# Kernel tuning notes

Hardware: AMD Instinct MI355X
Metric: run time of the kernel (lower is better)

Reference implementation:

```python
import jax, jax.numpy as jnp
import numpy as np

B = 16384      # batch
E = 128        # embed_dim
H = 256        # hidden_dim
OUT = 2        # output_dim
S = 32         # seq_length (decoder steps)
CAR = 8        # car_num


def setup_inputs() -> dict:
    key = jax.random.key(0)
    ks = jax.random.split(key, 17)
    def rn(k, shape, s=0.05):
        return jax.random.normal(k, shape, dtype=jnp.float32) * s
    return {
        "x": rn(ks[0], (B, 6 + CAR * 6), 1.0),
        "emb_mt_W": rn(ks[1], (E, 6)), "emb_mt_b": rn(ks[2], (E,)),
        "emb_v_W": rn(ks[3], (E, 6)), "emb_v_b": rn(ks[4], (E,)),
        "enc_Wih": rn(ks[5], (3 * H, E)), "enc_Whh": rn(ks[6], (3 * H, H)),
        "enc_bih": rn(ks[7], (3 * H,)), "enc_bhh": rn(ks[8], (3 * H,)),
        "dec_Wih": rn(ks[9], (3 * H, H)), "dec_Whh": rn(ks[10], (3 * H, H)),
        "dec_bih": rn(ks[11], (3 * H,)), "dec_bhh": rn(ks[12], (3 * H,)),
        "fc1_W": rn(ks[13], (H, H)), "fc1_b": rn(ks[14], (H,)),
        "fc2_W": rn(ks[15], (OUT, H)), "fc2_b": rn(ks[16], (OUT,)),
    }


def gru_cell(x, h, Wih, Whh, bih, bhh):
    # PyTorch GRU cell: r,z,n gate order
    gi = x @ Wih.T + bih          # [B, 3H]
    gh = h @ Whh.T + bhh          # [B, 3H]
    ir, iz, inn = jnp.split(gi, 3, axis=-1)
    hr, hz, hn = jnp.split(gh, 3, axis=-1)
    r = jax.nn.sigmoid(ir + hr)
    z = jax.nn.sigmoid(iz + hz)
    n = jnp.tanh(inn + r * hn)
    return (1.0 - z) * n + z * h


def reference(x, emb_mt_W, emb_mt_b, emb_v_W, emb_v_b,
              enc_Wih, enc_Whh, enc_bih, enc_bhh,
              dec_Wih, dec_Whh, dec_bih, dec_bhh,
              fc1_W, fc1_b, fc2_W, fc2_b):
    main_target = x[:, :6]                                  # [B,6]
    vehicles = x[:, 6:6 + CAR * 6].reshape(-1, CAR, 6)      # [B,CAR,6]
    # NOTE: original applies a random permutation over the CAR axis
    # (torch.randperm); we use the identity permutation for determinism,
    # the per-element math is identical.
    mt_emb = main_target @ emb_mt_W.T + emb_mt_b            # [B,E]
    v_emb = vehicles @ emb_v_W.T + emb_v_b                  # [B,CAR,E]
    seq = jnp.tanh(jnp.concatenate([v_emb, mt_emb[:, None, :]], axis=1))  # [B,CAR+1,E]

    h0 = jnp.zeros((x.shape[0], H), dtype=x.dtype)
    def enc_step(h, xt):
        return gru_cell(xt, h, enc_Wih, enc_Whh, enc_bih, enc_bhh), None
    h_enc, _ = jax.lax.scan(enc_step, h0, jnp.swapaxes(seq, 0, 1))  # [B,H]

    # decoder_input = encoder_output[:, -1] == final hidden (1-layer GRU)
    def dec_step(carry, _):
        dec_in, h = carry
        h = gru_cell(dec_in, h, dec_Wih, dec_Whh, dec_bih, dec_bhh)
        y = jnp.tanh(jax.nn.relu(h @ fc1_W.T + fc1_b) @ fc2_W.T + fc2_b)  # [B,OUT]
        return (h, h), y
    _, ys = jax.lax.scan(dec_step, (h_enc, h_enc), None, length=S)  # [S,B,OUT]
    return jnp.swapaxes(ys, 0, 1)  # [B,S,OUT]
```

## Files before the change

### kernel.cpp

```cpp
#include <hip/hip_runtime.h>
#include <math.h>
#include <stdint.h>

typedef _Float16 f16;
typedef _Float16 f16x8 __attribute__((ext_vector_type(8)));
typedef float    f32x16 __attribute__((ext_vector_type(16)));

#define NBLK 256
#define NTHR 512
#define MROW 64

#define ENCS 640
#define FC2S 1216
#define TOT_F 1232
#define TOT_E (TOT_F*512)

#define MFMA32(a,b,c) __builtin_amdgcn_mfma_f32_32x32x16_f16((a),(b),(c),0,0,0)
#define VMW4()  asm volatile("s_waitcnt vmcnt(4)" ::: "memory")
#define LGKM0() asm volatile("s_waitcnt lgkmcnt(0)" ::: "memory")
#define BARR()  do { __builtin_amdgcn_s_barrier(); asm volatile("" ::: "memory"); } while(0)

__device__ __forceinline__ void gld16(const f16* g, f16* lds){
  __builtin_amdgcn_global_load_lds(
      (const __attribute__((address_space(1))) void*)(uintptr_t)(const void*)g,
      (__attribute__((address_space(3))) void*)(uint32_t)(uintptr_t)(void*)lds,
      16, 0, 0);
}

__device__ __forceinline__ float sigm(float v){
  return __fdividef(1.0f, 1.0f + __expf(-v));
}
__device__ __forceinline__ float tanh_f(float v){
  float t = fminf(v, 8.0f);
  float e = __expf(2.0f * t);
  return 1.0f - 2.0f * __fdividef(1.0f, e + 1.0f);
}
__device__ __forceinline__ int eX(int row, int k){ return row*128 + (k ^ ((row & 7) << 3)); }

__global__ void prep_pack(const float* __restrict__ eWih, const float* __restrict__ eWhh,
                          const float* __restrict__ dWih, const float* __restrict__ dWhh,
                          const float* __restrict__ f1W,  const float* __restrict__ f2W,
                          f16* __restrict__ ws16)
{
  int idx = blockIdx.x * 256 + threadIdx.x;
  if (idx >= TOT_E) return;
  int frag = idx >> 9;
  int lo   = idx & 511;
  int l    = lo >> 3;
  int jj   = lo & 7;
  int c32  = l & 31;
  int half = l >> 5;
  int kin  = half*8 + jj;
  float v = 0.0f;
  if (frag < ENCS){
    int ct = frag / 80, r80 = frag % 80, n = r80 >> 1, j = r80 & 1;
    int col = ct*32 + c32;
    if (n < 16){ int k = n*16 + kin;
      v = (j == 0) ? (dWih[col*256 + k]       + dWhh[col*256 + k])
                   : (dWih[(256+col)*256 + k] + dWhh[(256+col)*256 + k]);
    } else if (n < 32){ int k = (n-16)*16 + kin;
      v = (j == 0) ? dWih[(512+col)*256 + k] : dWhh[(512+col)*256 + k];
    } else { int ks = (n-32)*2 + j; int k = ks*16 + kin;
      v = f1W[col*256 + k];
    }
  } else if (frag < FC2S){
    int f = frag - ENCS;
    int ct = f / 72, r = f % 72, n = r >> 1, j = r & 1;
    int col = ct*32 + c32;
    if (n < 8)       { int k = n*16 + kin;       v = eWih[(j*256 + col)*128 + k]; }
    else if (n < 24) { int k = (n-8)*16 + kin;   v = eWhh[(j*256 + col)*256 + k]; }
    else if (n < 28) { int ks = (n-24)*2 + j;    v = eWih[(512 + col)*128 + ks*16 + kin]; }
    else             { int ks = (n-28)*2 + j;    v = eWhh[(512 + col)*256 + ks*16 + kin]; }
  } else {
    int ks = frag - FC2S; int k = ks*16 + kin;
    v = (c32 < 2) ? f2W[c32*256 + k] : 0.0f;
  }
  ws16[idx] = (f16)v;
}

__global__ __launch_bounds__(NTHR, 1)
void fused_net(const float* __restrict__ x,
               const float* __restrict__ emW, const float* __restrict__ emb_,
               const float* __restrict__ evW, const float* __restrict__ evb,
               const float* __restrict__ ebih, const float* __restrict__ ebhh,
               const float* __restrict__ dbih, const float* __restrict__ dbhh,
               const float* __restrict__ f1b, const float* __restrict__ f2b,
               const f16* __restrict__ ws16, float* __restrict__ out)
{
  __shared__ __align__(16) f16 H0[16384];
  __shared__ __align__(16) f16 H1[16384];
  __shared__ __align__(16) f16 stg[32768];
  __shared__ __align__(16) f16 xbuf[8192];

  const int tid  = threadIdx.x;
  const int r0   = blockIdx.x * MROW;
  const int l    = tid & 63;
  const int wu   = __builtin_amdgcn_readfirstlane(tid >> 6);
  const int c32  = l & 31;
  const int half = l >> 5;
  const int lo8  = l << 3;

  f16* hp = H0;
  f16* hq = H1;

  const int abase = c32*256 + ((half*8) ^ ((l & 7) << 3));
  const int xab   = c32*128 + ((half*8) ^ ((l & 7) << 3));
  const int colm  = wu*32 + c32;

  f16* slot0 = stg + wu*4096;

  const f16* gdec = ws16 + (size_t)(wu*80)*512          + lo8;
  const f16* genc = ws16 + (size_t)(ENCS + wu*72)*512   + lo8;
  const f16* gfc2 = ws16 + (size_t)FC2S*512             + lo8;

  auto issue = [&](const f16* sb, int n, int q){
    f16* d = slot0 + q*1024;
    const f16* g = sb + (size_t)n*1024;
    gld16(g, d);
    gld16(g + 512, d + 512);
  };

  issue(genc, 0, 0); issue(genc, 1, 1); issue(genc, 2, 2);

  for (int i = tid; i < 16384; i += NTHR) H0[i] = (f16)0.0f;

  {
    const float ebr = ebih[colm]       + ebhh[colm];
    const float ebz = ebih[256 + colm] + ebhh[256 + colm];
    const float ebn = ebih[512 + colm];
    const float ebh = ebhh[512 + colm];

    #pragma unroll 1
    for (int t = 0; t < 9; ++t){
      const bool tlt8 = (t < 8);
      {
        int e  = tid & 127;
        int rq = tid >> 7;
        const float* Wp = tlt8 ? (evW + e*6) : (emW + e*6);
        float bb = tlt8 ? evb[e] : emb_[e];
        float w0 = Wp[0], w1 = Wp[1], w2 = Wp[2], w3 = Wp[3], w4 = Wp[4], w5 = Wp[5];
        int xo = tlt8 ? (6 + t*6) : 0;
        #pragma unroll 1
        for (int rr = 0; rr < 16; ++rr){
          int row = rq*16 + rr;
          const float* xs = x + (size_t)(r0 + row)*54 + xo;
          float a = bb + xs[0]*w0 + xs[1]*w1 + xs[2]*w2 + xs[3]*w3 + xs[4]*w4 + xs[5]*w5;
          xbuf[eX(row, e)] = (f16)tanh_f(a);
        }
      }
      LGKM0(); BARR();

      f32x16 rvv[2], zvv[2];
      {
        f32x16 aR[2], aZ[2];
        aR[0]=0.f; aR[1]=0.f; aZ[0]=0.f; aZ[1]=0.f;
        #pragma unroll 4
        for (int u = 0; u < 24; ++u){
          VMW4();
          issue(genc, u + 3, (u + 3) & 3);
          const f16* sp = slot0 + (u & 3)*1024;
          f16x8 b0 = *(const f16x8*)(sp + lo8);
          f16x8 b1 = *(const f16x8*)(sp + 512 + lo8);
          if (u < 8){
            int ao = xab ^ (u << 4);
            f16x8 a0 = *(const f16x8*)(xbuf + ao);
            f16x8 a1 = *(const f16x8*)(xbuf + ao + 4096);
            aR[0]=MFMA32(a0,b0,aR[0]); aR[1]=MFMA32(a1,b0,aR[1]);
            aZ[0]=MFMA32(a0,b1,aZ[0]); aZ[1]=MFMA32(a1,b1,aZ[1]);
          } else {
            int ao = abase ^ ((u - 8) << 4);
            f16x8 a0 = *(const f16x8*)(hp + ao);
            f16x8 a1 = *(const f16x8*)(hp + ao + 8192);
            aR[0]=MFMA32(a0,b0,aR[0]); aR[1]=MFMA32(a1,b0,aR[1]);
            aZ[0]=MFMA32(a0,b1,aZ[0]); aZ[1]=MFMA32(a1,b1,aZ[1]);
          }
        }
        #pragma unroll
        for (int rt = 0; rt < 2; ++rt)
          #pragma unroll
          for (int rg = 0; rg < 16; ++rg){
            rvv[rt][rg] = sigm(aR[rt][rg] + ebr);
            zvv[rt][rg] = sigm(aZ[rt][rg] + ebz);
          }
      }
      {
        f32x16 aN[2], aH[2];
        aN[0]=0.f; aN[1]=0.f; aH[0]=0.f; aH[1]=0.f;
        #pragma unroll
        for (int m = 0; m < 12; ++m){
          int u = 24 + m;
          VMW4();
          int nn = u + 3;
          if (nn < 36)      issue(genc, nn, nn & 3);
          else if (tlt8)    issue(genc, nn - 36, nn & 3);
          else              issue(gdec, nn - 36, nn & 3);
          const f16* sp = slot0 + (u & 3)*1024;
          f16x8 b0 = *(const f16x8*)(sp + lo8);
          f16x8 b1 = *(const f16x8*)(sp + 512 + lo8);
          if (m < 4){
            int j = 2*m;
            int ao0 = xab ^ (j << 4), ao1 = xab ^ ((j+1) << 4);
            f16x8 a0 = *(const f16x8*)(xbuf + ao0);
            f16x8 a1 = *(const f16x8*)(xbuf + ao0 + 4096);
            aN[0]=MFMA32(a0,b0,aN[0]); aN[1]=MFMA32(a1,b0,aN[1]);
            f16x8 a2 = *(const f16x8*)(xbuf + ao1);
            f16x8 a3 = *(const f16x8*)(xbuf + ao1 + 4096);
            aN[0]=MFMA32(a2,b1,aN[0]); aN[1]=MFMA32(a3,b1,aN[1]);
          } else {
            int k = 2*(m-4);
            int ao0 = abase ^ (k << 4), ao1 = abase ^ ((k+1) << 4);
            f16x8 a0 = *(const f16x8*)(hp + ao0);
            f16x8 a1 = *(const f16x8*)(hp + ao0 + 8192);
            aH[0]=MFMA32(a0,b0,aH[0]); aH[1]=MFMA32(a1,b0,aH[1]);
            f16x8 a2 = *(const f16x8*)(hp + ao1);
            f16x8 a3 = *(const f16x8*)(hp + ao1 + 8192);
            aH[0]=MFMA32(a2,b1,aH[0]); aH[1]=MFMA32(a3,b1,aH[1]);
          }
        }
        #pragma unroll
        for (int rt = 0; rt < 2; ++rt){
          #pragma unroll
          for (int rg = 0; rg < 16; ++rg){
            int rr  = (rg & 3) + 8*(rg >> 2) + 4*half;
            int row = rt*32 + rr;
            int el  = row*256 + (colm ^ ((rr & 7) << 3));
            float nv = tanh_f(aN[rt][rg] + ebn + rvv[rt][rg]*(aH[rt][rg] + ebh));
            float ho = (float)hp[el];
            hq[el] = (f16)(nv + zvv[rt][rg]*(ho - nv));
          }
        }
      }
      LGKM0(); BARR();
      { f16* tmp = hp; hp = hq; hq = tmp; }
    }
  }

  const float dbr = dbih[colm]       + dbhh[colm];
  const float dbz = dbih[256 + colm] + dbhh[256 + colm];
  const float dbn = dbih[512 + colm];
  const float dbh = dbhh[512 + colm];
  const float f1bb = f1b[colm];
  const float f2bb = (c32 < 2) ? f2b[c32] : 0.0f;

  #pragma unroll 1
  for (int s = 0; s < 32; ++s){
    f32x16 rvv[2], zvv[2];
    {
      f32x16 aR[2], aZ[2];
      aR[0]=0.f; aR[1]=0.f; aZ[0]=0.f; aZ[1]=0.f;
      #pragma unroll 4
      for (int u = 0; u < 16; ++u){
        VMW4();
        issue(gdec, u + 3, (u + 3) & 3);
        const f16* sp = slot0 + (u & 3)*1024;
        f16x8 b0 = *(const f16x8*)(sp + lo8);
        f16x8 b1 = *(const f16x8*)(sp + 512 + lo8);
        int ao = abase ^ (u << 4);
        f16x8 a0 = *(const f16x8*)(hp + ao);
        f16x8 a1 = *(const f16x8*)(hp + ao + 8192);
        aR[0]=MFMA32(a0,b0,aR[0]); aR[1]=MFMA32(a1,b0,aR[1]);
        aZ[0]=MFMA32(a0,b1,aZ[0]); aZ[1]=MFMA32(a1,b1,aZ[1]);
      }
      #pragma unroll
      for (int rt = 0; rt < 2; ++rt)
        #pragma unroll
        for (int rg = 0; rg < 16; ++rg){
          rvv[rt][rg] = sigm(aR[rt][rg] + dbr);
          zvv[rt][rg] = sigm(aZ[rt][rg] + dbz);
        }
    }
    BARR();

    {
      f32x16 aN[2], aH[2];
      aN[0]=0.f; aN[1]=0.f; aH[0]=0.f; aH[1]=0.f;
      #pragma unroll 4
      for (int u = 16; u < 32; ++u){
        VMW4();
        issue(gdec, u + 3, (u + 3) & 3);
        const f16* sp = slot0 + (u & 3)*1024;
        f16x8 b0 = *(const f16x8*)(sp + lo8);
        f16x8 b1 = *(const f16x8*)(sp + 512 + lo8);
        int k = u - 16;
        int ao = abase ^ (k << 4);
        f16x8 a0 = *(const f16x8*)(hp + ao);
        f16x8 a1 = *(const f16x8*)(hp + ao + 8192);
        aN[0]=MFMA32(a0,b0,aN[0]); aN[1]=MFMA32(a1,b0,aN[1]);
        aH[0]=MFMA32(a0,b1,aH[0]); aH[1]=MFMA32(a1,b1,aH[1]);
      }
      #pragma unroll
      for (int rt = 0; rt < 2; ++rt){
        #pragma unroll
        for (int rg = 0; rg < 16; ++rg){
          int rr  = (rg & 3) + 8*(rg >> 2) + 4*half;
          int row = rt*32 + rr;
          int el  = row*256 + (colm ^ ((rr & 7) << 3));
          float nv = tanh_f(aN[rt][rg] + dbn + rvv[rt][rg]*(aH[rt][rg] + dbh));
          float ho = (float)hp[el];
          hq[el] = (f16)(nv + zvv[rt][rg]*(ho - nv));
        }
      }
    }
    LGKM0(); BARR();

    {
      f32x16 aF[2];
      aF[0]=0.f; aF[1]=0.f;
      #pragma unroll
      for (int f = 0; f < 8; ++f){
        VMW4();
        int nn = 35 + f;
        if (nn < 40) issue(gdec, nn, nn & 3);
        else         issue(gdec, nn - 40, nn & 3);
        const f16* sp = slot0 + (f & 3)*1024;
        f16x8 b0 = *(const f16x8*)(sp + lo8);
        f16x8 b1 = *(const f16x8*)(sp + 512 + lo8);
        int k0 = 2*f;
        int ao0 = abase ^ (k0 << 4), ao1 = abase ^ ((k0+1) << 4);
        f16x8 a0 = *(const f16x8*)(hq + ao0);
        f16x8 a1 = *(const f16x8*)(hq + ao0 + 8192);
        aF[0]=MFMA32(a0,b0,aF[0]); aF[1]=MFMA32(a1,b0,aF[1]);
        f16x8 a2 = *(const f16x8*)(hq + ao1);
        f16x8 a3 = *(const f16x8*)(hq + ao1 + 8192);
        aF[0]=MFMA32(a2,b1,aF[0]); aF[1]=MFMA32(a3,b1,aF[1]);
      }
      #pragma unroll
      for (int rt = 0; rt < 2; ++rt){
        #pragma unroll
        for (int rg = 0; rg < 16; ++rg){
          int rr  = (rg & 3) + 8*(rg >> 2) + 4*half;
          int row = rt*32 + rr;
          int el  = row*256 + (colm ^ ((rr & 7) << 3));
          hp[el] = (f16)fmaxf(aF[rt][rg] + f1bb, 0.0f);
        }
      }
    }
    LGKM0(); BARR();

    if (wu < 2){
      f32x16 a2 = 0.f;
      const int rb = wu * 8192;
      #pragma unroll
      for (int ks = 0; ks < 16; ++ks){
        f16x8 bv = *(const f16x8*)(gfc2 + (size_t)ks*512);
        f16x8 a0 = *(const f16x8*)(hp + ((abase + rb) ^ (ks << 4)));
        a2 = MFMA32(a0, bv, a2);
      }
      if (c32 < 2){
        #pragma unroll
        for (int rg = 0; rg < 16; ++rg){
          int rr = (rg & 3) + 8*(rg >> 2) + 4*half;
          out[((size_t)(r0 + wu*32 + rr)*32 + s)*2 + c32] = tanh_f(a2[rg] + f2bb);
        }
      }
    }
    { f16* tmp = hp; hp = hq; hq = tmp; }
  }
}

extern "C" void kernel_launch(void* const* d_in, const int* in_sizes, int n_in,
                              void* d_out, int out_size, void* d_ws, size_t ws_size,
                              hipStream_t stream)
{
  (void)in_sizes; (void)n_in; (void)out_size; (void)ws_size;
  const float* x    = (const float*)d_in[0];
  const float* emW  = (const float*)d_in[1];
  const float* emb_ = (const float*)d_in[2];
  const float* evW  = (const float*)d_in[3];
  const float* evb  = (const float*)d_in[4];
  const float* eWih = (const float*)d_in[5];
  const float* eWhh = (const float*)d_in[6];
  const float* ebih = (const float*)d_in[7];
  const float* ebhh = (const float*)d_in[8];
  const float* dWih = (const float*)d_in[9];
  const float* dWhh = (const float*)d_in[10];
  const float* dbih = (const float*)d_in[11];
  const float* dbhh = (const float*)d_in[12];
  const float* f1W  = (const float*)d_in[13];
  const float* f1b  = (const float*)d_in[14];
  const float* f2W  = (const float*)d_in[15];
  const float* f2b  = (const float*)d_in[16];
  float* out = (float*)d_out;
  f16* ws16 = (f16*)d_ws;

  prep_pack<<<(TOT_E + 255)/256, 256, 0, stream>>>(eWih, eWhh, dWih, dWhh, f1W, f2W, ws16);
  fused_net<<<NBLK, NTHR, 0, stream>>>(x, emW, emb_, evW, evb, ebih, ebhh,
                                       dbih, dbhh, f1b, f2b, ws16, out);
}
```

Before: 748.4 us.

## Halve rows per block, shrink LDS, triple-buffer weight staging for multi-block occupancy

Rows per block go from 64 to 32 and the grid doubles to 512 blocks, with launch bounds raised so several blocks can share a CU. LDS use shrinks: the hidden buffers are halved, the separate x buffer is dropped by reusing the spare hidden buffer for embedded inputs, and the weight staging ring goes from four slots to three with a rotating pointer set. Each MFMA step now uses a single 32-row accumulator, and the next weight slice is issued only after the LDS reads (lgkmcnt wait). The intent is to hide latency through more resident waves. The cost is that every block now streams the full weight set for half as many rows, so weight traffic through L2 doubles, and the extra barrier in the encoder step plus the three-slot rotation add synchronization hazards.

New measurement: 2.341 ms. 3.13x slower.

```diff
diff --git a/kernel.cpp b/kernel.cpp
--- a/kernel.cpp
+++ b/kernel.cpp
@@ -6,9 +6,9 @@
 typedef _Float16 f16x8 __attribute__((ext_vector_type(8)));
 typedef float    f32x16 __attribute__((ext_vector_type(16)));
 
-#define NBLK 256
+#define NBLK 512
 #define NTHR 512
-#define MROW 64
+#define MROW 32
 
 #define ENCS 640
 #define FC2S 1216
@@ -78,7 +78,7 @@
   ws16[idx] = (f16)v;
 }
 
-__global__ __launch_bounds__(NTHR, 1)
+__global__ __launch_bounds__(NTHR, 4)
 void fused_net(const float* __restrict__ x,
                const float* __restrict__ emW, const float* __restrict__ emb_,
                const float* __restrict__ evW, const float* __restrict__ evb,
@@ -87,10 +87,9 @@
                const float* __restrict__ f1b, const float* __restrict__ f2b,
                const f16* __restrict__ ws16, float* __restrict__ out)
 {
-  __shared__ __align__(16) f16 H0[16384];
-  __shared__ __align__(16) f16 H1[16384];
-  __shared__ __align__(16) f16 stg[32768];
-  __shared__ __align__(16) f16 xbuf[8192];
+  __shared__ __align__(16) f16 H0[8192];
+  __shared__ __align__(16) f16 H1[8192];
+  __shared__ __align__(16) f16 stg[24576];
 
   const int tid  = threadIdx.x;
   const int r0   = blockIdx.x * MROW;
@@ -107,22 +106,22 @@
   const int xab   = c32*128 + ((half*8) ^ ((l & 7) << 3));
   const int colm  = wu*32 + c32;
 
-  f16* slot0 = stg + wu*4096;
+  f16* spp[3];
+  spp[0] = stg + wu*3072;
+  spp[1] = spp[0] + 1024;
+  spp[2] = spp[0] + 2048;
 
   const f16* gdec = ws16 + (size_t)(wu*80)*512          + lo8;
   const f16* genc = ws16 + (size_t)(ENCS + wu*72)*512   + lo8;
   const f16* gfc2 = ws16 + (size_t)FC2S*512             + lo8;
 
-  auto issue = [&](const f16* sb, int n, int q){
-    f16* d = slot0 + q*1024;
-    const f16* g = sb + (size_t)n*1024;
-    gld16(g, d);
-    gld16(g + 512, d + 512);
-  };
-
-  issue(genc, 0, 0); issue(genc, 1, 1); issue(genc, 2, 2);
-
-  for (int i = tid; i < 16384; i += NTHR) H0[i] = (f16)0.0f;
+  {
+    gld16(genc,            spp[0]); gld16(genc + 512,           spp[0] + 512);
+    gld16(genc + 1024,     spp[1]); gld16(genc + 1536,          spp[1] + 512);
+    gld16(genc + 2048,     spp[2]); gld16(genc + 2560,          spp[2] + 512);
+  }
+
+  for (int i = tid; i < 8192; i += NTHR) H0[i] = (f16)0.0f;
 
   {
     const float ebr = ebih[colm]       + ebhh[colm];
@@ -133,6 +132,7 @@
     #pragma unroll 1
     for (int t = 0; t < 9; ++t){
       const bool tlt8 = (t < 8);
+      f16* xb = hq;
       {
         int e  = tid & 127;
         int rq = tid >> 7;
@@ -141,93 +141,86 @@
         float w0 = Wp[0], w1 = Wp[1], w2 = Wp[2], w3 = Wp[3], w4 = Wp[4], w5 = Wp[5];
         int xo = tlt8 ? (6 + t*6) : 0;
         #pragma unroll 1
-        for (int rr = 0; rr < 16; ++rr){
-          int row = rq*16 + rr;
+        for (int rr = 0; rr < 8; ++rr){
+          int row = rq*8 + rr;
           const float* xs = x + (size_t)(r0 + row)*54 + xo;
           float a = bb + xs[0]*w0 + xs[1]*w1 + xs[2]*w2 + xs[3]*w3 + xs[4]*w4 + xs[5]*w5;
-          xbuf[eX(row, e)] = (f16)tanh_f(a);
+          xb[eX(row, e)] = (f16)tanh_f(a);
         }
       }
       LGKM0(); BARR();
 
-      f32x16 rvv[2], zvv[2];
+      f32x16 rvv, zvv;
       {
-        f32x16 aR[2], aZ[2];
-        aR[0]=0.f; aR[1]=0.f; aZ[0]=0.f; aZ[1]=0.f;
-        #pragma unroll 4
+        f32x16 aR = 0.f, aZ = 0.f;
+        #pragma unroll
         for (int u = 0; u < 24; ++u){
           VMW4();
-          issue(genc, u + 3, (u + 3) & 3);
-          const f16* sp = slot0 + (u & 3)*1024;
+          f16* sp = spp[u % 3];
           f16x8 b0 = *(const f16x8*)(sp + lo8);
           f16x8 b1 = *(const f16x8*)(sp + 512 + lo8);
-          if (u < 8){
-            int ao = xab ^ (u << 4);
-            f16x8 a0 = *(const f16x8*)(xbuf + ao);
-            f16x8 a1 = *(const f16x8*)(xbuf + ao + 4096);
-            aR[0]=MFMA32(a0,b0,aR[0]); aR[1]=MFMA32(a1,b0,aR[1]);
-            aZ[0]=MFMA32(a0,b1,aZ[0]); aZ[1]=MFMA32(a1,b1,aZ[1]);
-          } else {
-            int ao = abase ^ ((u - 8) << 4);
-            f16x8 a0 = *(const f16x8*)(hp + ao);
-            f16x8 a1 = *(const f16x8*)(hp + ao + 8192);
-            aR[0]=MFMA32(a0,b0,aR[0]); aR[1]=MFMA32(a1,b0,aR[1]);
-            aZ[0]=MFMA32(a0,b1,aZ[0]); aZ[1]=MFMA32(a1,b1,aZ[1]);
-          }
-        }
-        #pragma unroll
-        for (int rt = 0; rt < 2; ++rt)
-          #pragma unroll
-          for (int rg = 0; rg < 16; ++rg){
-            rvv[rt][rg] = sigm(aR[rt][rg] + ebr);
-            zvv[rt][rg] = sigm(aZ[rt][rg] + ebz);
-          }
-      }
+          f16x8 a0 = (u < 8) ? *(const f16x8*)(xb + (xab ^ (u << 4)))
+                             : *(const f16x8*)(hp + (abase ^ ((u - 8) << 4)));
+          LGKM0();
+          { const f16* g = genc + (size_t)(u + 3)*1024;
+            gld16(g, sp); gld16(g + 512, sp + 512); }
+          aR = MFMA32(a0, b0, aR);
+          aZ = MFMA32(a0, b1, aZ);
+        }
+        #pragma unroll
+        for (int rg = 0; rg < 16; ++rg){
+          rvv[rg] = sigm(aR[rg] + ebr);
+          zvv[rg] = sigm(aZ[rg] + ebz);
+        }
+      }
+      f32x16 aN = 0.f, aH = 0.f;
       {
-        f32x16 aN[2], aH[2];
-        aN[0]=0.f; aN[1]=0.f; aH[0]=0.f; aH[1]=0.f;
-        #pragma unroll
-        for (int m = 0; m < 12; ++m){
+        #pragma unroll
+        for (int m = 0; m < 4; ++m){
           int u = 24 + m;
           VMW4();
-          int nn = u + 3;
-          if (nn < 36)      issue(genc, nn, nn & 3);
-          else if (tlt8)    issue(genc, nn - 36, nn & 3);
-          else              issue(gdec, nn - 36, nn & 3);
-          const f16* sp = slot0 + (u & 3)*1024;
+          f16* sp = spp[u % 3];
           f16x8 b0 = *(const f16x8*)(sp + lo8);
           f16x8 b1 = *(const f16x8*)(sp + 512 + lo8);
-          if (m < 4){
-            int j = 2*m;
-            int ao0 = xab ^ (j << 4), ao1 = xab ^ ((j+1) << 4);
-            f16x8 a0 = *(const f16x8*)(xbuf + ao0);
-            f16x8 a1 = *(const f16x8*)(xbuf + ao0 + 4096);
-            aN[0]=MFMA32(a0,b0,aN[0]); aN[1]=MFMA32(a1,b0,aN[1]);
-            f16x8 a2 = *(const f16x8*)(xbuf + ao1);
-            f16x8 a3 = *(const f16x8*)(xbuf + ao1 + 4096);
-            aN[0]=MFMA32(a2,b1,aN[0]); aN[1]=MFMA32(a3,b1,aN[1]);
-          } else {
-            int k = 2*(m-4);
-            int ao0 = abase ^ (k << 4), ao1 = abase ^ ((k+1) << 4);
-            f16x8 a0 = *(const f16x8*)(hp + ao0);
-            f16x8 a1 = *(const f16x8*)(hp + ao0 + 8192);
-            aH[0]=MFMA32(a0,b0,aH[0]); aH[1]=MFMA32(a1,b0,aH[1]);
-            f16x8 a2 = *(const f16x8*)(hp + ao1);
-            f16x8 a3 = *(const f16x8*)(hp + ao1 + 8192);
-            aH[0]=MFMA32(a2,b1,aH[0]); aH[1]=MFMA32(a3,b1,aH[1]);
-          }
-        }
-        #pragma unroll
-        for (int rt = 0; rt < 2; ++rt){
-          #pragma unroll
-          for (int rg = 0; rg < 16; ++rg){
-            int rr  = (rg & 3) + 8*(rg >> 2) + 4*half;
-            int row = rt*32 + rr;
-            int el  = row*256 + (colm ^ ((rr & 7) << 3));
-            float nv = tanh_f(aN[rt][rg] + ebn + rvv[rt][rg]*(aH[rt][rg] + ebh));
-            float ho = (float)hp[el];
-            hq[el] = (f16)(nv + zvv[rt][rg]*(ho - nv));
-          }
+          int j = 2*m;
+          f16x8 a0 = *(const f16x8*)(xb + (xab ^ (j << 4)));
+          f16x8 a1 = *(const f16x8*)(xb + (xab ^ ((j + 1) << 4)));
+          LGKM0();
+          { const f16* g = genc + (size_t)(u + 3)*1024;
+            gld16(g, sp); gld16(g + 512, sp + 512); }
+          aN = MFMA32(a0, b0, aN);
+          aN = MFMA32(a1, b1, aN);
+        }
+      }
+      LGKM0(); BARR();
+      {
+        #pragma unroll
+        for (int m = 4; m < 12; ++m){
+          int u = 24 + m;
+          VMW4();
+          f16* sp = spp[u % 3];
+          f16x8 b0 = *(const f16x8*)(sp + lo8);
+          f16x8 b1 = *(const f16x8*)(sp + 512 + lo8);
+          int k = 2*(m - 4);
+          f16x8 a0 = *(const f16x8*)(hp + (abase ^ (k << 4)));
+          f16x8 a1 = *(const f16x8*)(hp + (abase ^ ((k + 1) << 4)));
+          LGKM0();
+          { int nn = u + 3;
+            const f16* g;
+            if (nn < 36)      g = genc + (size_t)nn*1024;
+            else if (tlt8)    g = genc + (size_t)(nn - 36)*1024;
+            else              g = gdec + (size_t)(nn - 36)*1024;
+            gld16(g, sp); gld16(g + 512, sp + 512); }
+          aH = MFMA32(a0, b0, aH);
+          aH = MFMA32(a1, b1, aH);
+        }
+        #pragma unroll
+        for (int rg = 0; rg < 16; ++rg){
+          int rr = (rg & 3) + 8*(rg >> 2) + 4*half;
+          int el = rr*256 + (colm ^ ((rr & 7) << 3));
+          float nv = tanh_f(aN[rg] + ebn + rvv[rg]*(aH[rg] + ebh));
+          float ho = (float)hp[el];
+          hq[el] = (f16)(nv + zvv[rg]*(ho - nv));
         }
       }
       LGKM0(); BARR();
@@ -244,116 +237,99 @@
 
   #pragma unroll 1
   for (int s = 0; s < 32; ++s){
-    f32x16 rvv[2], zvv[2];
+    f32x16 rvv, zvv;
     {
-      f32x16 aR[2], aZ[2];
-      aR[0]=0.f; aR[1]=0.f; aZ[0]=0.f; aZ[1]=0.f;
-      #pragma unroll 4
+      f32x16 aR = 0.f, aZ = 0.f;
+      #pragma unroll
       for (int u = 0; u < 16; ++u){
         VMW4();
-        issue(gdec, u + 3, (u + 3) & 3);
-        const f16* sp = slot0 + (u & 3)*1024;
+        f16* sp = spp[u % 3];
         f16x8 b0 = *(const f16x8*)(sp + lo8);
         f16x8 b1 = *(const f16x8*)(sp + 512 + lo8);
-        int ao = abase ^ (u << 4);
-        f16x8 a0 = *(const f16x8*)(hp + ao);
-        f16x8 a1 = *(const f16x8*)(hp + ao + 8192);
-        aR[0]=MFMA32(a0,b0,aR[0]); aR[1]=MFMA32(a1,b0,aR[1]);
-        aZ[0]=MFMA32(a0,b1,aZ[0]); aZ[1]=MFMA32(a1,b1,aZ[1]);
-      }
-      #pragma unroll
-      for (int rt = 0; rt < 2; ++rt)
-        #pragma unroll
-        for (int rg = 0; rg < 16; ++rg){
-          rvv[rt][rg] = sigm(aR[rt][rg] + dbr);
-          zvv[rt][rg] = sigm(aZ[rt][rg] + dbz);
-        }
+        f16x8 a0 = *(const f16x8*)(hp + (abase ^ (u << 4)));
+        LGKM0();
+        { const f16* g = gdec + (size_t)(u + 3)*1024;
+          gld16(g, sp); gld16(g + 512, sp + 512); }
+        aR = MFMA32(a0, b0, aR);
+        aZ = MFMA32(a0, b1, aZ);
+      }
+      #pragma unroll
+      for (int rg = 0; rg < 16; ++rg){
+        rvv[rg] = sigm(aR[rg] + dbr);
+        zvv[rg] = sigm(aZ[rg] + dbz);
+      }
     }
     BARR();
 
     {
-      f32x16 aN[2], aH[2];
-      aN[0]=0.f; aN[1]=0.f; aH[0]=0.f; aH[1]=0.f;
-      #pragma unroll 4
+      f32x16 aN = 0.f, aH = 0.f;
+      #pragma unroll
       for (int u = 16; u < 32; ++u){
         VMW4();
-        issue(gdec, u + 3, (u + 3) & 3);
-        const f16* sp = slot0 + (u & 3)*1024;
+        f16* sp = spp[u % 3];
         f16x8 b0 = *(const f16x8*)(sp + lo8);
         f16x8 b1 = *(const f16x8*)(sp + 512 + lo8);
-        int k = u - 16;
-        int ao = abase ^ (k << 4);
-        f16x8 a0 = *(const f16x8*)(hp + ao);
-        f16x8 a1 = *(const f16x8*)(hp + ao + 8192);
-        aN[0]=MFMA32(a0,b0,aN[0]); aN[1]=MFMA32(a1,b0,aN[1]);
-        aH[0]=MFMA32(a0,b1,aH[0]); aH[1]=MFMA32(a1,b1,aH[1]);
-      }
-      #pragma unroll
-      for (int rt = 0; rt < 2; ++rt){
-        #pragma unroll
-        for (int rg = 0; rg < 16; ++rg){
-          int rr  = (rg & 3) + 8*(rg >> 2) + 4*half;
-          int row = rt*32 + rr;
-          int el  = row*256 + (colm ^ ((rr & 7) << 3));
-          float nv = tanh_f(aN[rt][rg] + dbn + rvv[rt][rg]*(aH[rt][rg] + dbh));
-          float ho = (float)hp[el];
-          hq[el] = (f16)(nv + zvv[rt][rg]*(ho - nv));
-        }
+        f16x8 a0 = *(const f16x8*)(hp + (abase ^ ((u - 16) << 4)));
+        LGKM0();
+        { const f16* g = gdec + (size_t)(u + 3)*1024;
+          gld16(g, sp); gld16(g + 512, sp + 512); }
+        aN = MFMA32(a0, b0, aN);
+        aH = MFMA32(a0, b1, aH);
+      }
+      #pragma unroll
+      for (int rg = 0; rg < 16; ++rg){
+        int rr = (rg & 3) + 8*(rg >> 2) + 4*half;
+        int el = rr*256 + (colm ^ ((rr & 7) << 3));
+        float nv = tanh_f(aN[rg] + dbn + rvv[rg]*(aH[rg] + dbh));
+        float ho = (float)hp[el];
+        hq[el] = (f16)(nv + zvv[rg]*(ho - nv));
       }
     }
     LGKM0(); BARR();
 
     {
-      f32x16 aF[2];
-      aF[0]=0.f; aF[1]=0.f;
-      #pragma unroll
-      for (int f = 0; f < 8; ++f){
+      f32x16 aF = 0.f;
+      #pragma unroll
+      for (int u = 32; u < 40; ++u){
         VMW4();
-        int nn = 35 + f;
-        if (nn < 40) issue(gdec, nn, nn & 3);
-        else         issue(gdec, nn - 40, nn & 3);
-        const f16* sp = slot0 + (f & 3)*1024;
+        f16* sp = spp[u % 3];
         f16x8 b0 = *(const f16x8*)(sp + lo8);
         f16x8 b1 = *(const f16x8*)(sp + 512 + lo8);
-        int k0 = 2*f;
-        int ao0 = abase ^ (k0 << 4), ao1 = abase ^ ((k0+1) << 4);
-        f16x8 a0 = *(const f16x8*)(hq + ao0);
-        f16x8 a1 = *(const f16x8*)(hq + ao0 + 8192);
-        aF[0]=MFMA32(a0,b0,aF[0]); aF[1]=MFMA32(a1,b0,aF[1]);
-        f16x8 a2 = *(const f16x8*)(hq + ao1);
-        f16x8 a3 = *(const f16x8*)(hq + ao1 + 8192);
-        aF[0]=MFMA32(a2,b1,aF[0]); aF[1]=MFMA32(a3,b1,aF[1]);
-      }
-      #pragma unroll
-      for (int rt = 0; rt < 2; ++rt){
-        #pragma unroll
-        for (int rg = 0; rg < 16; ++rg){
-          int rr  = (rg & 3) + 8*(rg >> 2) + 4*half;
-          int row = rt*32 + rr;
-          int el  = row*256 + (colm ^ ((rr & 7) << 3));
-          hp[el] = (f16)fmaxf(aF[rt][rg] + f1bb, 0.0f);
-        }
+        int k0 = 2*(u - 32);
+        f16x8 a0 = *(const f16x8*)(hq + (abase ^ (k0 << 4)));
+        f16x8 a1 = *(const f16x8*)(hq + (abase ^ ((k0 + 1) << 4)));
+        LGKM0();
+        { const f16* g = gdec + (size_t)((u + 3) % 40)*1024;
+          gld16(g, sp); gld16(g + 512, sp + 512); }
+        aF = MFMA32(a0, b0, aF);
+        aF = MFMA32(a1, b1, aF);
+      }
+      #pragma unroll
+      for (int rg = 0; rg < 16; ++rg){
+        int rr = (rg & 3) + 8*(rg >> 2) + 4*half;
+        int el = rr*256 + (colm ^ ((rr & 7) << 3));
+        hp[el] = (f16)fmaxf(aF[rg] + f1bb, 0.0f);
       }
     }
     LGKM0(); BARR();
 
-    if (wu < 2){
+    if (wu == 0){
       f32x16 a2 = 0.f;
-      const int rb = wu * 8192;
       #pragma unroll
       for (int ks = 0; ks < 16; ++ks){
         f16x8 bv = *(const f16x8*)(gfc2 + (size_t)ks*512);
-        f16x8 a0 = *(const f16x8*)(hp + ((abase + rb) ^ (ks << 4)));
+        f16x8 a0 = *(const f16x8*)(hp + (abase ^ (ks << 4)));
         a2 = MFMA32(a0, bv, a2);
       }
       if (c32 < 2){
         #pragma unroll
         for (int rg = 0; rg < 16; ++rg){
           int rr = (rg & 3) + 8*(rg >> 2) + 4*half;
-          out[((size_t)(r0 + wu*32 + rr)*32 + s)*2 + c32] = tanh_f(a2[rg] + f2bb);
-        }
-      }
-    }
+          out[((size_t)(r0 + rr)*32 + s)*2 + c32] = tanh_f(a2[rg] + f2bb);
+        }
+      }
+    }
+    { f16* t0 = spp[0]; spp[0] = spp[1]; spp[1] = spp[2]; spp[2] = t0; }
     { f16* tmp = hp; hp = hq; hq = tmp; }
   }
 }
```

## Deepen weight staging to five slots, pair K-steps, widen LDS swizzle, reuse hq for x

Applied to the files above, without the earlier changes.

Switches the per-wave weight staging ring from four slots to five and processes two K-slices per wait, issuing two prefetches per iteration so more global-to-LDS loads are in flight. Each wait now covers two slices, with the ring rotating across encoder steps. The LDS XOR swizzle widens from 8 to 16 row groups to cut bank conflicts. The separate x buffer is removed and embeddings are written into the idle hq buffer, which adds a barrier before the h-dependent n-gate work. Fully unrolling the loops raises register and code pressure, and the pointer-array ring rotation adds complexity.

Result: slower. 1.838 ms (+145.6%).

```diff
diff --git a/kernel.cpp b/kernel.cpp
--- a/kernel.cpp
+++ b/kernel.cpp
@@ -35,7 +35,7 @@
   float e = __expf(2.0f * t);
   return 1.0f - 2.0f * __fdividef(1.0f, e + 1.0f);
 }
-__device__ __forceinline__ int eX(int row, int k){ return row*128 + (k ^ ((row & 7) << 3)); }
+__device__ __forceinline__ int eX(int row, int k){ return row*128 + (k ^ ((row & 15) << 3)); }
 
 __global__ void prep_pack(const float* __restrict__ eWih, const float* __restrict__ eWhh,
                           const float* __restrict__ dWih, const float* __restrict__ dWhh,
@@ -89,8 +89,7 @@
 {
   __shared__ __align__(16) f16 H0[16384];
   __shared__ __align__(16) f16 H1[16384];
-  __shared__ __align__(16) f16 stg[32768];
-  __shared__ __align__(16) f16 xbuf[8192];
+  __shared__ __align__(16) f16 stg[40960];
 
   const int tid  = threadIdx.x;
   const int r0   = blockIdx.x * MROW;
@@ -103,24 +102,24 @@
   f16* hp = H0;
   f16* hq = H1;
 
-  const int abase = c32*256 + ((half*8) ^ ((l & 7) << 3));
-  const int xab   = c32*128 + ((half*8) ^ ((l & 7) << 3));
+  const int abase = c32*256 + ((half*8) ^ ((l & 15) << 3));
+  const int xab   = c32*128 + ((half*8) ^ ((l & 15) << 3));
   const int colm  = wu*32 + c32;
 
-  f16* slot0 = stg + wu*4096;
+  f16* spp[5];
+  #pragma unroll
+  for (int i = 0; i < 5; ++i) spp[i] = stg + wu*5120 + i*1024;
 
   const f16* gdec = ws16 + (size_t)(wu*80)*512          + lo8;
   const f16* genc = ws16 + (size_t)(ENCS + wu*72)*512   + lo8;
   const f16* gfc2 = ws16 + (size_t)FC2S*512             + lo8;
 
-  auto issue = [&](const f16* sb, int n, int q){
-    f16* d = slot0 + q*1024;
-    const f16* g = sb + (size_t)n*1024;
-    gld16(g, d);
-    gld16(g + 512, d + 512);
-  };
-
-  issue(genc, 0, 0); issue(genc, 1, 1); issue(genc, 2, 2);
+  auto issue2 = [&](const f16* g, f16* d){ gld16(g, d); gld16(g + 512, d + 512); };
+
+  issue2(genc,        spp[0]);
+  issue2(genc + 1024, spp[1]);
+  issue2(genc + 2048, spp[2]);
+  issue2(genc + 3072, spp[3]);
 
   for (int i = tid; i < 16384; i += NTHR) H0[i] = (f16)0.0f;
 
@@ -133,6 +132,7 @@
     #pragma unroll 1
     for (int t = 0; t < 9; ++t){
       const bool tlt8 = (t < 8);
+      f16* xb = hq;
       {
         int e  = tid & 127;
         int rq = tid >> 7;
@@ -145,7 +145,7 @@
           int row = rq*16 + rr;
           const float* xs = x + (size_t)(r0 + row)*54 + xo;
           float a = bb + xs[0]*w0 + xs[1]*w1 + xs[2]*w2 + xs[3]*w3 + xs[4]*w4 + xs[5]*w5;
-          xbuf[eX(row, e)] = (f16)tanh_f(a);
+          xb[eX(row, e)] = (f16)tanh_f(a);
         }
       }
       LGKM0(); BARR();
@@ -154,25 +154,36 @@
       {
         f32x16 aR[2], aZ[2];
         aR[0]=0.f; aR[1]=0.f; aZ[0]=0.f; aZ[1]=0.f;
-        #pragma unroll 4
-        for (int u = 0; u < 24; ++u){
+        #pragma unroll
+        for (int p = 0; p < 12; ++p){
+          const int u0 = 2*p, u1 = 2*p + 1;
           VMW4();
-          issue(genc, u + 3, (u + 3) & 3);
-          const f16* sp = slot0 + (u & 3)*1024;
-          f16x8 b0 = *(const f16x8*)(sp + lo8);
-          f16x8 b1 = *(const f16x8*)(sp + 512 + lo8);
-          if (u < 8){
-            int ao = xab ^ (u << 4);
-            f16x8 a0 = *(const f16x8*)(xbuf + ao);
-            f16x8 a1 = *(const f16x8*)(xbuf + ao + 4096);
-            aR[0]=MFMA32(a0,b0,aR[0]); aR[1]=MFMA32(a1,b0,aR[1]);
-            aZ[0]=MFMA32(a0,b1,aZ[0]); aZ[1]=MFMA32(a1,b1,aZ[1]);
-          } else {
-            int ao = abase ^ ((u - 8) << 4);
-            f16x8 a0 = *(const f16x8*)(hp + ao);
-            f16x8 a1 = *(const f16x8*)(hp + ao + 8192);
-            aR[0]=MFMA32(a0,b0,aR[0]); aR[1]=MFMA32(a1,b0,aR[1]);
-            aZ[0]=MFMA32(a0,b1,aZ[0]); aZ[1]=MFMA32(a1,b1,aZ[1]);
+          f16* s0 = spp[u0 % 5];
+          f16* s1 = spp[u1 % 5];
+          f16x8 b00 = *(const f16x8*)(s0 + lo8);
+          f16x8 b01 = *(const f16x8*)(s0 + 512 + lo8);
+          f16x8 b10 = *(const f16x8*)(s1 + lo8);
+          f16x8 b11 = *(const f16x8*)(s1 + 512 + lo8);
+          issue2(genc + (size_t)(u0 + 4)*1024, spp[(u0 + 4) % 5]);
+          issue2(genc + (size_t)(u1 + 4)*1024, spp[(u1 + 4) % 5]);
+          #pragma unroll
+          for (int q = 0; q < 2; ++q){
+            const int u = q ? u1 : u0;
+            f16x8 b0 = q ? b10 : b00;
+            f16x8 b1 = q ? b11 : b01;
+            if (u < 8){
+              int ao = xab ^ (u << 4);
+              f16x8 a0 = *(const f16x8*)(xb + ao);
+              f16x8 a1 = *(const f16x8*)(xb + ao + 4096);
+              aR[0]=MFMA32(a0,b0,aR[0]); aR[1]=MFMA32(a1,b0,aR[1]);
+              aZ[0]=MFMA32(a0,b1,aZ[0]); aZ[1]=MFMA32(a1,b1,aZ[1]);
+            } else {
+              int ao = abase ^ ((u - 8) << 4);
+              f16x8 a0 = *(const f16x8*)(hp + ao);
+              f16x8 a1 = *(const f16x8*)(hp + ao + 8192);
+              aR[0]=MFMA32(a0,b0,aR[0]); aR[1]=MFMA32(a1,b0,aR[1]);
+              aZ[0]=MFMA32(a0,b1,aZ[0]); aZ[1]=MFMA32(a1,b1,aZ[1]);
+            }
           }
         }
         #pragma unroll
@@ -183,31 +194,64 @@
             zvv[rt][rg] = sigm(aZ[rt][rg] + ebz);
           }
       }
+      f32x16 aN[2], aH[2];
+      aN[0]=0.f; aN[1]=0.f; aH[0]=0.f; aH[1]=0.f;
       {
-        f32x16 aN[2], aH[2];
-        aN[0]=0.f; aN[1]=0.f; aH[0]=0.f; aH[1]=0.f;
-        #pragma unroll
-        for (int m = 0; m < 12; ++m){
-          int u = 24 + m;
+        #pragma unroll
+        for (int p = 12; p < 14; ++p){
+          const int u0 = 2*p, u1 = 2*p + 1;
           VMW4();
-          int nn = u + 3;
-          if (nn < 36)      issue(genc, nn, nn & 3);
-          else if (tlt8)    issue(genc, nn - 36, nn & 3);
-          else              issue(gdec, nn - 36, nn & 3);
-          const f16* sp = slot0 + (u & 3)*1024;
-          f16x8 b0 = *(const f16x8*)(sp + lo8);
-          f16x8 b1 = *(const f16x8*)(sp + 512 + lo8);
-          if (m < 4){
+          f16* s0 = spp[u0 % 5];
+          f16* s1 = spp[u1 % 5];
+          f16x8 b00 = *(const f16x8*)(s0 + lo8);
+          f16x8 b01 = *(const f16x8*)(s0 + 512 + lo8);
+          f16x8 b10 = *(const f16x8*)(s1 + lo8);
+          f16x8 b11 = *(const f16x8*)(s1 + 512 + lo8);
+          issue2(genc + (size_t)(u0 + 4)*1024, spp[(u0 + 4) % 5]);
+          issue2(genc + (size_t)(u1 + 4)*1024, spp[(u1 + 4) % 5]);
+          #pragma unroll
+          for (int q = 0; q < 2; ++q){
+            const int m = (q ? u1 : u0) - 24;
+            f16x8 b0 = q ? b10 : b00;
+            f16x8 b1 = q ? b11 : b01;
             int j = 2*m;
             int ao0 = xab ^ (j << 4), ao1 = xab ^ ((j+1) << 4);
-            f16x8 a0 = *(const f16x8*)(xbuf + ao0);
-            f16x8 a1 = *(const f16x8*)(xbuf + ao0 + 4096);
+            f16x8 a0 = *(const f16x8*)(xb + ao0);
+            f16x8 a1 = *(const f16x8*)(xb + ao0 + 4096);
             aN[0]=MFMA32(a0,b0,aN[0]); aN[1]=MFMA32(a1,b0,aN[1]);
-            f16x8 a2 = *(const f16x8*)(xbuf + ao1);
-            f16x8 a3 = *(const f16x8*)(xbuf + ao1 + 4096);
+            f16x8 a2 = *(const f16x8*)(xb + ao1);
+            f16x8 a3 = *(const f16x8*)(xb + ao1 + 4096);
             aN[0]=MFMA32(a2,b1,aN[0]); aN[1]=MFMA32(a3,b1,aN[1]);
-          } else {
-            int k = 2*(m-4);
+          }
+        }
+      }
+      LGKM0(); BARR();
+      {
+        #pragma unroll
+        for (int p = 14; p < 18; ++p){
+          const int u0 = 2*p, u1 = 2*p + 1;
+          VMW4();
+          f16* s0 = spp[u0 % 5];
+          f16* s1 = spp[u1 % 5];
+          f16x8 b00 = *(const f16x8*)(s0 + lo8);
+          f16x8 b01 = *(const f16x8*)(s0 + 512 + lo8);
+          f16x8 b10 = *(const f16x8*)(s1 + lo8);
+          f16x8 b11 = *(const f16x8*)(s1 + 512 + lo8);
+          {
+            const int n0 = u0 + 4, n1 = u1 + 4;
+            const f16* g0 = (n0 < 36) ? (genc + (size_t)n0*1024)
+                                      : ((tlt8 ? genc : gdec) + (size_t)(n0 - 36)*1024);
+            const f16* g1 = (n1 < 36) ? (genc + (size_t)n1*1024)
+                                      : ((tlt8 ? genc : gdec) + (size_t)(n1 - 36)*1024);
+            issue2(g0, spp[n0 % 5]);
+            issue2(g1, spp[n1 % 5]);
+          }
+          #pragma unroll
+          for (int q = 0; q < 2; ++q){
+            const int m = (q ? u1 : u0) - 24;
+            f16x8 b0 = q ? b10 : b00;
+            f16x8 b1 = q ? b11 : b01;
+            int k = 2*(m - 4);
             int ao0 = abase ^ (k << 4), ao1 = abase ^ ((k+1) << 4);
             f16x8 a0 = *(const f16x8*)(hp + ao0);
             f16x8 a1 = *(const f16x8*)(hp + ao0 + 8192);
@@ -223,7 +267,7 @@
           for (int rg = 0; rg < 16; ++rg){
             int rr  = (rg & 3) + 8*(rg >> 2) + 4*half;
             int row = rt*32 + rr;
-            int el  = row*256 + (colm ^ ((rr & 7) << 3));
+            int el  = row*256 + (colm ^ ((rr & 15) << 3));
             float nv = tanh_f(aN[rt][rg] + ebn + rvv[rt][rg]*(aH[rt][rg] + ebh));
             float ho = (float)hp[el];
             hq[el] = (f16)(nv + zvv[rt][rg]*(ho - nv));
@@ -232,6 +276,7 @@
       }
       LGKM0(); BARR();
       { f16* tmp = hp; hp = hq; hq = tmp; }
+      { f16* t0 = spp[0]; spp[0]=spp[1]; spp[1]=spp[2]; spp[2]=spp[3]; spp[3]=spp[4]; spp[4]=t0; }
     }
   }
 
@@ -248,18 +293,29 @@
     {
       f32x16 aR[2], aZ[2];
       aR[0]=0.f; aR[1]=0.f; aZ[0]=0.f; aZ[1]=0.f;
-      #pragma unroll 4
-      for (int u = 0; u < 16; ++u){
+      #pragma unroll
+      for (int p = 0; p < 8; ++p){
+        const int u0 = 2*p, u1 = 2*p + 1;
         VMW4();
-        issue(gdec, u + 3, (u + 3) & 3);
-        const f16* sp = slot0 + (u & 3)*1024;
-        f16x8 b0 = *(const f16x8*)(sp + lo8);
-        f16x8 b1 = *(const f16x8*)(sp + 512 + lo8);
-        int ao = abase ^ (u << 4);
-        f16x8 a0 = *(const f16x8*)(hp + ao);
-        f16x8 a1 = *(const f16x8*)(hp + ao + 8192);
-        aR[0]=MFMA32(a0,b0,aR[0]); aR[1]=MFMA32(a1,b0,aR[1]);
-        aZ[0]=MFMA32(a0,b1,aZ[0]); aZ[1]=MFMA32(a1,b1,aZ[1]);
+        f16* s0 = spp[u0 % 5];
+        f16* s1 = spp[u1 % 5];
+        f16x8 b00 = *(const f16x8*)(s0 + lo8);
+        f16x8 b01 = *(const f16x8*)(s0 + 512 + lo8);
+        f16x8 b10 = *(const f16x8*)(s1 + lo8);
+        f16x8 b11 = *(const f16x8*)(s1 + 512 + lo8);
+        issue2(gdec + (size_t)(u0 + 4)*1024, spp[(u0 + 4) % 5]);
+        issue2(gdec + (size_t)(u1 + 4)*1024, spp[(u1 + 4) % 5]);
+        #pragma unroll
+        for (int q = 0; q < 2; ++q){
+          const int u = q ? u1 : u0;
+          f16x8 b0 = q ? b10 : b00;
+          f16x8 b1 = q ? b11 : b01;
+          int ao = abase ^ (u << 4);
+          f16x8 a0 = *(const f16x8*)(hp + ao);
+          f16x8 a1 = *(const f16x8*)(hp + ao + 8192);
+          aR[0]=MFMA32(a0,b0,aR[0]); aR[1]=MFMA32(a1,b0,aR[1]);
+          aZ[0]=MFMA32(a0,b1,aZ[0]); aZ[1]=MFMA32(a1,b1,aZ[1]);
+        }
       }
       #pragma unroll
       for (int rt = 0; rt < 2; ++rt)
@@ -274,19 +330,29 @@
     {
       f32x16 aN[2], aH[2];
       aN[0]=0.f; aN[1]=0.f; aH[0]=0.f; aH[1]=0.f;
-      #pragma unroll 4
-      for (int u = 16; u < 32; ++u){
+      #pragma unroll
+      for (int p = 8; p < 16; ++p){
+        const int u0 = 2*p, u1 = 2*p + 1;
         VMW4();
-        issue(gdec, u + 3, (u + 3) & 3);
-        const f16* sp = slot0 + (u & 3)*1024;
-        f16x8 b0 = *(const f16x8*)(sp + lo8);
-        f16x8 b1 = *(const f16x8*)(sp + 512 + lo8);
-        int k = u - 16;
-        int ao = abase ^ (k << 4);
-        f16x8 a0 = *(const f16x8*)(hp + ao);
-        f16x8 a1 = *(const f16x8*)(hp + ao + 8192);
-        aN[0]=MFMA32(a0,b0,aN[0]); aN[1]=MFMA32(a1,b0,aN[1]);
-        aH[0]=MFMA32(a0,b1,aH[0]); aH[1]=MFMA32(a1,b1,aH[1]);
+        f16* s0 = spp[u0 % 5];
+        f16* s1 = spp[u1 % 5];
+        f16x8 b00 = *(const f16x8*)(s0 + lo8);
+        f16x8 b01 = *(const f16x8*)(s0 + 512 + lo8);
+        f16x8 b10 = *(const f16x8*)(s1 + lo8);
+        f16x8 b11 = *(const f16x8*)(s1 + 512 + lo8);
+        issue2(gdec + (size_t)(u0 + 4)*1024, spp[(u0 + 4) % 5]);
+        issue2(gdec + (size_t)(u1 + 4)*1024, spp[(u1 + 4) % 5]);
+        #pragma unroll
+        for (int q = 0; q < 2; ++q){
+          const int u = q ? u1 : u0;
+          f16x8 b0 = q ? b10 : b00;
+          f16x8 b1 = q ? b11 : b01;
+          int ao = abase ^ ((u - 16) << 4);
+          f16x8 a0 = *(const f16x8*)(hp + ao);
+          f16x8 a1 = *(const f16x8*)(hp + ao + 8192);
+          aN[0]=MFMA32(a0,b0,aN[0]); aN[1]=MFMA32(a1,b0,aN[1]);
+          aH[0]=MFMA32(a0,b1,aH[0]); aH[1]=MFMA32(a1,b1,aH[1]);
+        }
       }
       #pragma unroll
       for (int rt = 0; rt < 2; ++rt){
@@ -294,7 +360,7 @@
         for (int rg = 0; rg < 16; ++rg){
           int rr  = (rg & 3) + 8*(rg >> 2) + 4*half;
           int row = rt*32 + rr;
-          int el  = row*256 + (colm ^ ((rr & 7) << 3));
+          int el  = row*256 + (colm ^ ((rr & 15) << 3));
           float nv = tanh_f(aN[rt][rg] + dbn + rvv[rt][rg]*(aH[rt][rg] + dbh));
           float ho = (float)hp[el];
           hq[el] = (f16)(nv + zvv[rt][rg]*(ho - nv));
@@ -307,22 +373,36 @@
       f32x16 aF[2];
       aF[0]=0.f; aF[1]=0.f;
       #pragma unroll
-      for (int f = 0; f < 8; ++f){
+      for (int p = 16; p < 20; ++p){
+        const int u0 = 2*p, u1 = 2*p + 1;
         VMW4();
-        int nn = 35 + f;
-        if (nn < 40) issue(gdec, nn, nn & 3);
-        else         issue(gdec, nn - 40, nn & 3);
-        const f16* sp = slot0 + (f & 3)*1024;
-        f16x8 b0 = *(const f16x8*)(sp + lo8);
-        f16x8 b1 = *(const f16x8*)(sp + 512 + lo8);
-        int k0 = 2*f;
-        int ao0 = abase ^ (k0 << 4), ao1 = abase ^ ((k0+1) << 4);
-        f16x8 a0 = *(const f16x8*)(hq + ao0);
-        f16x8 a1 = *(const f16x8*)(hq + ao0 + 8192);
-        aF[0]=MFMA32(a0,b0,aF[0]); aF[1]=MFMA32(a1,b0,aF[1]);
-        f16x8 a2 = *(const f16x8*)(hq + ao1);
-        f16x8 a3 = *(const f16x8*)(hq + ao1 + 8192);
-        aF[0]=MFMA32(a2,b1,aF[0]); aF[1]=MFMA32(a3,b1,aF[1]);
+        f16* s0 = spp[u0 % 5];
+        f16* s1 = spp[u1 % 5];
+        f16x8 b00 = *(const f16x8*)(s0 + lo8);
+        f16x8 b01 = *(const f16x8*)(s0 + 512 + lo8);
+        f16x8 b10 = *(const f16x8*)(s1 + lo8);
+        f16x8 b11 = *(const f16x8*)(s1 + 512 + lo8);
+        {
+          const int n0 = u0 + 4, n1 = u1 + 4;
+          const f16* g0 = gdec + (size_t)(n0 < 40 ? n0 : n0 - 40)*1024;
+          const f16* g1 = gdec + (size_t)(n1 < 40 ? n1 : n1 - 40)*1024;
+          issue2(g0, spp[n0 % 5]);
+          issue2(g1, spp[n1 % 5]);
+        }
+        #pragma unroll
+        for (int q = 0; q < 2; ++q){
+          const int f = (q ? u1 : u0) - 32;
+          f16x8 b0 = q ? b10 : b00;
+          f16x8 b1 = q ? b11 : b01;
+          int k0 = 2*f;
+          int ao0 = abase ^ (k0 << 4), ao1 = abase ^ ((k0+1) << 4);
+          f16x8 a0 = *(const f16x8*)(hq + ao0);
+          f16x8 a1 = *(const f16x8*)(hq + ao0 + 8192);
+          aF[0]=MFMA32(a0,b0,aF[0]); aF[1]=MFMA32(a1,b0,aF[1]);
+          f16x8 a2 = *(const f16x8*)(hq + ao1);
+          f16x8 a3 = *(const f16x8*)(hq + ao1 + 8192);
+          aF[0]=MFMA32(a2,b1,aF[0]); aF[1]=MFMA32(a3,b1,aF[1]);
+        }
       }
       #pragma unroll
       for (int rt = 0; rt < 2; ++rt){
@@ -330,7 +410,7 @@
         for (int rg = 0; rg < 16; ++rg){
           int rr  = (rg & 3) + 8*(rg >> 2) + 4*half;
           int row = rt*32 + rr;
-          int el  = row*256 + (colm ^ ((rr & 7) << 3));
+          int el  = row*256 + (colm ^ ((rr & 15) << 3));
           hp[el] = (f16)fmaxf(aF[rt][rg] + f1bb, 0.0f);
         }
       }
```
